# Optimization experiments

Measured on AMD Instinct MI355X. Metric: run time of the kernel, lower is better.

## Reference

```python
import jax, jax.numpy as jnp
import numpy as np

B, S, D, H, Dh, F = 1, 2048, 2048, 24, 128, 8192  # batch, seq, dim, heads, dim_head, ff hidden
SCALE = Dh ** -0.5


def _layernorm(x, g, b, eps=1e-5):
    mu = jnp.mean(x, axis=-1, keepdims=True)
    var = jnp.var(x, axis=-1, keepdims=True)
    return (x - mu) * jax.lax.rsqrt(var + eps) * g + b


def _rmsnorm(x, g, eps=1e-5):
    ms = jnp.mean(jnp.square(x), axis=-1, keepdims=True)
    return x * jax.lax.rsqrt(ms + eps) * g


def setup_inputs() -> dict:
    key = jax.random.key(0)
    ks = jax.random.split(key, 8)
    w = lambda k, sh: (jax.random.normal(k, sh, jnp.float32) * (1.0 / np.sqrt(sh[0]))).astype(jnp.float32)
    return {
        "x": jax.random.normal(ks[0], (B, S, D), jnp.float32),
        "ln_g": jnp.ones((D,), jnp.float32),
        "ln_b": jnp.zeros((D,), jnp.float32),
        "attn_g": jnp.ones((D,), jnp.float32),  # RingAttention prenorm (RMSNorm) gamma
        "Wq": w(ks[1], (D, H * Dh)),
        "Wk": w(ks[2], (D, H * Dh)),
        "Wv": w(ks[3], (D, H * Dh)),
        "Wo": w(ks[4], (H * Dh, D)),
        "W1": w(ks[5], (D, F)),
        "b1": jnp.zeros((F,), jnp.float32),
        "W2": w(ks[6], (F, D)),
        "b2": jnp.zeros((D,), jnp.float32),
    }


def reference(x, ln_g, ln_b, attn_g, Wq, Wk, Wv, Wo, W1, b1, W2, b2):
    # outer block LayerNorm
    x = _layernorm(x, ln_g, ln_b)

    # --- causal multi-head attention (math-equivalent to ring attention) ---
    h = _rmsnorm(x, attn_g)  # attention's internal prenorm
    q = (h @ Wq).reshape(B, S, H, Dh)
    k = (h @ Wk).reshape(B, S, H, Dh)
    v = (h @ Wv).reshape(B, S, H, Dh)
    scores = jnp.einsum("bqhd,bkhd->bhqk", q, k) * SCALE  # [B,H,S,S]
    causal = jnp.tril(jnp.ones((S, S), bool))
    scores = jnp.where(causal, scores, jnp.finfo(scores.dtype).min)
    attn = jax.nn.softmax(scores, axis=-1)
    o = jnp.einsum("bhqk,bkhd->bqhd", attn, v).reshape(B, S, H * Dh)
    x = o @ Wo + x  # residual

    # --- feedforward + residual ---
    x = jax.nn.gelu(x @ W1 + b1) @ W2 + b2 + x
    return x
```

## Files before the change

kernel.cpp:

```cpp
#include <hip/hip_runtime.h>
#include <hip/hip_bf16.h>

#define Sq 2048
#define Dm 2048
#define HDim 3072
#define QKVDim 9216
#define NH 24
#define DH 128
#define FF 8192
#define ATT_SCALE 0.08838834764831845f

using bf16 = __hip_bfloat16;
typedef __attribute__((ext_vector_type(8))) short bf16x8;
typedef __attribute__((ext_vector_type(4))) float f32x4;
typedef unsigned int u32;
typedef unsigned long long u64;
typedef __attribute__((ext_vector_type(4))) u32 u32x4;

__device__ __forceinline__ void gload_lds16(const void* g, void* l) {
    __builtin_amdgcn_global_load_lds(
        (const __attribute__((address_space(1))) void*)g,
        (__attribute__((address_space(3))) void*)l, 16, 0, 0);
}

__global__ __launch_bounds__(256) void ln_rms_kernel(
    const float* __restrict__ x, const float* __restrict__ g, const float* __restrict__ b,
    const float* __restrict__ ag, float* __restrict__ xnf, bf16* __restrict__ h)
{
    __shared__ float redA[4], redB[4], redC[4];
    int row = blockIdx.x;
    int t = threadIdx.x;
    int lane = t & 63, wid = t >> 6;
    const float* xr = x + (size_t)row * Dm;

    float v[8];
    float sum = 0.f, ssq = 0.f;
#pragma unroll
    for (int i = 0; i < 8; i++) {
        float f = xr[t + 256 * i];
        v[i] = f; sum += f; ssq += f * f;
    }
#pragma unroll
    for (int off = 32; off > 0; off >>= 1) {
        sum += __shfl_down(sum, off);
        ssq += __shfl_down(ssq, off);
    }
    if (lane == 0) { redA[wid] = sum; redB[wid] = ssq; }
    __syncthreads();
    sum = redA[0] + redA[1] + redA[2] + redA[3];
    ssq = redB[0] + redB[1] + redB[2] + redB[3];
    float mu = sum * (1.f / Dm);
    float var = ssq * (1.f / Dm) - mu * mu;
    float rstd = rsqrtf(var + 1e-5f);

    float xn[8];
    float s2 = 0.f;
#pragma unroll
    for (int i = 0; i < 8; i++) {
        int col = t + 256 * i;
        float xv = (v[i] - mu) * rstd * g[col] + b[col];
        xn[i] = xv;
        xnf[(size_t)row * Dm + col] = xv;
        s2 += xv * xv;
    }
#pragma unroll
    for (int off = 32; off > 0; off >>= 1) s2 += __shfl_down(s2, off);
    if (lane == 0) redC[wid] = s2;
    __syncthreads();
    s2 = redC[0] + redC[1] + redC[2] + redC[3];
    float rms = rsqrtf(s2 * (1.f / Dm) + 1e-5f);
#pragma unroll
    for (int i = 0; i < 8; i++) {
        int col = t + 256 * i;
        h[(size_t)row * Dm + col] = __float2bfloat16(xn[i] * rms * ag[col]);
    }
}

__global__ __launch_bounds__(256) void transpose_cvt_kernel(
    const float* __restrict__ W, bf16* __restrict__ Wt, int K, int N)
{
    __shared__ float tile[32][36];
    int n0 = blockIdx.x * 32, k0 = blockIdx.y * 32;
    int t = threadIdx.x;
    int r = t >> 3, c4 = (t & 7) * 4;
    f32x4 v = *reinterpret_cast<const f32x4*>(W + (size_t)(k0 + r) * N + n0 + c4);
    *reinterpret_cast<f32x4*>(&tile[r][c4]) = v;
    __syncthreads();
    int nr = t >> 3, kc = (t & 7) * 4;
    bf16 o4[4];
    o4[0] = __float2bfloat16(tile[kc + 0][nr]);
    o4[1] = __float2bfloat16(tile[kc + 1][nr]);
    o4[2] = __float2bfloat16(tile[kc + 2][nr]);
    o4[3] = __float2bfloat16(tile[kc + 3][nr]);
    *reinterpret_cast<u64*>(Wt + (size_t)(n0 + nr) * K + k0 + kc) = *reinterpret_cast<const u64*>(o4);
}

__global__ __launch_bounds__(256) void transpose_cvt3_kernel(
    const float* __restrict__ Wa, const float* __restrict__ Wb, const float* __restrict__ Wc,
    bf16* __restrict__ Wt, int K, int N)
{
    __shared__ float tile[32][36];
    const float* W = blockIdx.z == 0 ? Wa : (blockIdx.z == 1 ? Wb : Wc);
    bf16* dst = Wt + (size_t)blockIdx.z * N * K;
    int n0 = blockIdx.x * 32, k0 = blockIdx.y * 32;
    int t = threadIdx.x;
    int r = t >> 3, c4 = (t & 7) * 4;
    f32x4 v = *reinterpret_cast<const f32x4*>(W + (size_t)(k0 + r) * N + n0 + c4);
    *reinterpret_cast<f32x4*>(&tile[r][c4]) = v;
    __syncthreads();
    int nr = t >> 3, kc = (t & 7) * 4;
    bf16 o4[4];
    o4[0] = __float2bfloat16(tile[kc + 0][nr]);
    o4[1] = __float2bfloat16(tile[kc + 1][nr]);
    o4[2] = __float2bfloat16(tile[kc + 2][nr]);
    o4[3] = __float2bfloat16(tile[kc + 3][nr]);
    *reinterpret_cast<u64*>(dst + (size_t)(n0 + nr) * K + k0 + kc) = *reinterpret_cast<const u64*>(o4);
}

__global__ __launch_bounds__(256) void cvt_prefill_kernel(
    const float* __restrict__ xnf, const float* __restrict__ bias,
    bf16* __restrict__ hb, float* __restrict__ o, int N)
{
    int i = (blockIdx.x * 256 + threadIdx.x) * 8;
    int col = i % N;
    f32x4 a = *reinterpret_cast<const f32x4*>(xnf + i);
    f32x4 b = *reinterpret_cast<const f32x4*>(xnf + i + 4);
    bf16 r[8];
#pragma unroll
    for (int j = 0; j < 4; j++) { r[j] = __float2bfloat16(a[j]); r[4 + j] = __float2bfloat16(b[j]); }
    *reinterpret_cast<u32x4*>(hb + i) = *reinterpret_cast<const u32x4*>(r);
    f32x4 b0 = *reinterpret_cast<const f32x4*>(bias + col);
    f32x4 b1v = *reinterpret_cast<const f32x4*>(bias + col + 4);
    f32x4 o0 = {a[0] + b0[0], a[1] + b0[1], a[2] + b0[2], a[3] + b0[3]};
    f32x4 o1 = {b[0] + b1v[0], b[1] + b1v[1], b[2] + b1v[2], b[3] + b1v[3]};
    *reinterpret_cast<f32x4*>(o + i) = o0;
    *reinterpret_cast<f32x4*>(o + i + 4) = o1;
}

template <int EPI>
__global__ __launch_bounds__(256, 4) void gemm_kernel(
    const bf16* __restrict__ A, const bf16* __restrict__ Bt,
    int M, int N, int K, int Ksplit,
    bf16* Cb, float* Cf, const float* __restrict__ bias)
{
    __shared__ __align__(16) bf16 As[128 * 64];
    __shared__ __align__(16) bf16 Bs[128 * 64];
    int m0 = blockIdx.y * 128, n0 = blockIdx.x * 128;
    int kbeg = blockIdx.z * Ksplit, kend = kbeg + Ksplit;
    int tid = threadIdx.x;
    int lane = tid & 63, w = tid >> 6;
    int wr = w >> 1, wc = w & 1;
    int l15 = lane & 15, lhi = lane >> 4;

    int srow = lane >> 3;
    int scol = ((lane & 7) ^ (lane >> 3)) * 8;

    const f32x4 zero4 = {0.f, 0.f, 0.f, 0.f};
    f32x4 acc[4][4];
#pragma unroll
    for (int m = 0; m < 4; m++)
#pragma unroll
        for (int n = 0; n < 4; n++) acc[m][n] = zero4;

    for (int k0 = kbeg; k0 < kend; k0 += 64) {
        __syncthreads();
#pragma unroll
        for (int c = 0; c < 4; c++) {
            int row = w * 32 + c * 8 + srow;
            gload_lds16(A + (size_t)(m0 + row) * K + k0 + scol,
                        (char*)As + w * 4096 + c * 1024);
            gload_lds16(Bt + (size_t)(n0 + row) * K + k0 + scol,
                        (char*)Bs + w * 4096 + c * 1024);
        }
        __syncthreads();
#pragma unroll
        for (int ks = 0; ks < 2; ks++) {
            bf16x8 af[4], bfr[4];
#pragma unroll
            for (int m = 0; m < 4; m++) {
                int r = wr * 64 + m * 16 + l15;
                af[m] = *reinterpret_cast<const bf16x8*>(
                    &As[r * 64 + (((ks << 2) + lhi) ^ (r & 7)) * 8]);
            }
#pragma unroll
            for (int n = 0; n < 4; n++) {
                int r = wc * 64 + n * 16 + l15;
                bfr[n] = *reinterpret_cast<const bf16x8*>(
                    &Bs[r * 64 + (((ks << 2) + lhi) ^ (r & 7)) * 8]);
            }
#pragma unroll
            for (int m = 0; m < 4; m++)
#pragma unroll
                for (int n = 0; n < 4; n++)
                    acc[m][n] = __builtin_amdgcn_mfma_f32_16x16x32_bf16(af[m], bfr[n], acc[m][n], 0, 0, 0);
        }
    }

#pragma unroll
    for (int m = 0; m < 4; m++) {
        int row = m0 + wr * 64 + m * 16 + lhi * 4;
#pragma unroll
        for (int n = 0; n < 4; n++) {
            int col = n0 + wc * 64 + n * 16 + l15;
#pragma unroll
            for (int j = 0; j < 4; j++) {
                float vv = acc[m][n][j];
                size_t idx = (size_t)(row + j) * N + col;
                if (EPI == 0) {
                    Cb[idx] = __float2bfloat16(vv);
                } else if (EPI == 2) {
                    float o = vv + bias[col];
                    float u = 1.5957691216057308f * (o + 0.044715f * o * o * o);
                    Cb[idx] = __float2bfloat16(o / (1.0f + __expf(-u)));
                } else {
                    atomicAdd(&Cf[idx], vv);
                }
            }
        }
    }
}

__global__ __launch_bounds__(256) void attn_kernel(
    const bf16* __restrict__ qkv, bf16* __restrict__ o)
{
    __shared__ __align__(16) bf16 KsF[2][64 * 128];
    __shared__ __align__(16) bf16 VtF[2][128 * 72];
    __shared__ __align__(16) bf16 Pl[4][16][72];
    int rank = blockIdx.x;
    int qb = (Sq / 128 - 1) - rank / NH;
    int head = rank % NH;
    const bf16* q = qkv + head * DH;
    const bf16* k = qkv + HDim + head * DH;
    const bf16* v = qkv + 2 * HDim + head * DH;
    int tid = threadIdx.x, lane = tid & 63, w = tid >> 6;
    int l15 = lane & 15, lhi = lane >> 4;

    bf16x8 aq[2][4];
#pragma unroll
    for (int s = 0; s < 2; s++) {
        const bf16* qbase = q + (size_t)(qb * 128 + s * 64 + w * 16 + l15) * QKVDim;
#pragma unroll
        for (int kk = 0; kk < 4; kk++)
            aq[s][kk] = *reinterpret_cast<const bf16x8*>(qbase + kk * 32 + lhi * 8);
    }

    int krow_st = w * 16;
    int vkv = lhi * 2 + (w & 1) + (w >> 1) * 8;
    int vd0 = l15 * 8;
    int vxr = l15 & 7;

    const f32x4 zero4 = {0.f, 0.f, 0.f, 0.f};
    f32x4 acc_o[2][8];
    float mrow[2][4], lrow[2][4];
#pragma unroll
    for (int s = 0; s < 2; s++) {
#pragma unroll
        for (int db = 0; db < 8; db++) acc_o[s][db] = zero4;
#pragma unroll
        for (int r = 0; r < 4; r++) { mrow[s][r] = -1e30f; lrow[s][r] = 0.f; }
    }

    int nt = 2 * qb + 2;

    {
#pragma unroll
        for (int c = 0; c < 4; c++) {
            int row = krow_st + c * 4 + lhi;
            int cb = l15 ^ (row & 7);
            gload_lds16(k + (size_t)row * QKVDim + cb * 8,
                        (char*)&KsF[0][0] + w * 4096 + c * 1024);
        }
#pragma unroll
        for (int i = 0; i < 4; i++) {
            int kv = vkv + i * 16;
            bf16x8 vv = *reinterpret_cast<const bf16x8*>(v + (size_t)kv * QKVDim + vd0);
            int vb = kv >> 3, kr = kv & 7;
#pragma unroll
            for (int j = 0; j < 8; j++)
                VtF[0][(vd0 + j) * 72 + ((vb ^ vxr) << 3) + kr] = ((const bf16*)&vv)[j];
        }
        asm volatile("s_waitcnt vmcnt(0)" ::: "memory");
        __syncthreads();
    }

    for (int kb = 0; kb < nt; kb++) {
        int kv0 = kb * 64;
        int p = kb & 1;
        bf16x8 vreg[4];
        bool pref = (kb + 1 < nt);
        if (pref) {
            int nv0 = kv0 + 64;
#pragma unroll
            for (int c = 0; c < 4; c++) {
                int row = krow_st + c * 4 + lhi;
                int cb = l15 ^ (row & 7);
                gload_lds16(k + (size_t)(nv0 + row) * QKVDim + cb * 8,
                            (char*)&KsF[p ^ 1][0] + w * 4096 + c * 1024);
            }
#pragma unroll
            for (int i = 0; i < 4; i++) {
                int kv = vkv + i * 16;
                vreg[i] = *reinterpret_cast<const bf16x8*>(v + (size_t)(nv0 + kv) * QKVDim + vd0);
            }
        }

#pragma unroll
        for (int s = 0; s < 2; s++) {
            int qr0s = qb * 128 + s * 64 + w * 16;
            if (kv0 > qr0s + 15) continue;

            f32x4 sacc[4];
#pragma unroll
            for (int nb = 0; nb < 4; nb++) {
                sacc[nb] = zero4;
                int krow = nb * 16 + l15;
#pragma unroll
                for (int kk = 0; kk < 4; kk++) {
                    const char* kp = (const char*)&KsF[p][0] + krow * 256 +
                                     ((kk * 64 + lhi * 16) ^ ((krow & 7) << 4));
                    bf16x8 bk = *reinterpret_cast<const bf16x8*>(kp);
                    sacc[nb] = __builtin_amdgcn_mfma_f32_16x16x32_bf16(aq[s][kk], bk, sacc[nb], 0, 0, 0);
                }
            }

            bool msk = (kv0 + 63 > qr0s);
            float sv[4][4];
            float pm[4];
#pragma unroll
            for (int r = 0; r < 4; r++) pm[r] = -1e30f;
#pragma unroll
            for (int nb = 0; nb < 4; nb++) {
                int kvc = kv0 + nb * 16 + l15;
#pragma unroll
                for (int r = 0; r < 4; r++) {
                    int qr = qr0s + lhi * 4 + r;
                    float ss = sacc[nb][r] * ATT_SCALE;
                    if (msk && kvc > qr) ss = -1e30f;
                    sv[nb][r] = ss;
                    pm[r] = fmaxf(pm[r], ss);
                }
            }
#pragma unroll
            for (int off = 1; off < 16; off <<= 1)
#pragma unroll
                for (int r = 0; r < 4; r++)
                    pm[r] = fmaxf(pm[r], __shfl_xor(pm[r], off));

            float ls[4];
#pragma unroll
            for (int r = 0; r < 4; r++) {
                float mnew = fmaxf(mrow[s][r], pm[r]);
                float sc = __expf(mrow[s][r] - mnew);
                mrow[s][r] = mnew;
                lrow[s][r] *= sc;
#pragma unroll
                for (int db = 0; db < 8; db++) acc_o[s][db][r] *= sc;
                float lsr = 0.f;
#pragma unroll
                for (int nb = 0; nb < 4; nb++) {
                    float pp = __expf(sv[nb][r] - mnew);
                    sv[nb][r] = pp;
                    lsr += pp;
                }
                ls[r] = lsr;
            }
#pragma unroll
            for (int off = 1; off < 16; off <<= 1)
#pragma unroll
                for (int r = 0; r < 4; r++)
                    ls[r] += __shfl_xor(ls[r], off);
#pragma unroll
            for (int r = 0; r < 4; r++) lrow[s][r] += ls[r];

#pragma unroll
            for (int nb = 0; nb < 4; nb++)
#pragma unroll
                for (int r = 0; r < 4; r++)
                    Pl[w][lhi * 4 + r][nb * 16 + l15] = __float2bfloat16(sv[nb][r]);

#pragma unroll
            for (int ks = 0; ks < 2; ks++) {
                bf16x8 ap = *reinterpret_cast<const bf16x8*>(&Pl[w][l15][ks * 32 + lhi * 8]);
#pragma unroll
                for (int db = 0; db < 8; db++) {
                    int dv = db * 16 + l15;
                    int blk = (ks * 4 + lhi) ^ ((dv >> 3) & 7);
                    bf16x8 bv = *reinterpret_cast<const bf16x8*>(&VtF[p][dv * 72 + blk * 8]);
                    acc_o[s][db] = __builtin_amdgcn_mfma_f32_16x16x32_bf16(ap, bv, acc_o[s][db], 0, 0, 0);
                }
            }
        }

        __syncthreads();
        if (pref) {
            int nv0 = kv0 + 64;
            (void)nv0;
#pragma unroll
            for (int i = 0; i < 4; i++) {
                int kv = vkv + i * 16;
                int vb = kv >> 3, kr = kv & 7;
#pragma unroll
                for (int j = 0; j < 8; j++)
                    VtF[p ^ 1][(vd0 + j) * 72 + ((vb ^ vxr) << 3) + kr] = ((const bf16*)&vreg[i])[j];
            }
            asm volatile("s_waitcnt vmcnt(0)" ::: "memory");
            __syncthreads();
        }
    }

#pragma unroll
    for (int s = 0; s < 2; s++)
#pragma unroll
        for (int db = 0; db < 8; db++)
#pragma unroll
            for (int r = 0; r < 4; r++) {
                int qr = qb * 128 + s * 64 + w * 16 + lhi * 4 + r;
                float val = acc_o[s][db][r] / lrow[s][r];
                o[(size_t)qr * HDim + head * DH + db * 16 + l15] = __float2bfloat16(val);
            }
}

extern "C" void kernel_launch(void* const* d_in, const int* in_sizes, int n_in,
                              void* d_out, int out_size, void* d_ws, size_t ws_size,
                              hipStream_t stream)
{
    const float* x     = (const float*)d_in[0];
    const float* ln_g  = (const float*)d_in[1];
    const float* ln_b  = (const float*)d_in[2];
    const float* attng = (const float*)d_in[3];
    const float* Wq    = (const float*)d_in[4];
    const float* Wk    = (const float*)d_in[5];
    const float* Wv    = (const float*)d_in[6];
    const float* Wo    = (const float*)d_in[7];
    const float* W1    = (const float*)d_in[8];
    const float* b1    = (const float*)d_in[9];
    const float* W2    = (const float*)d_in[10];
    const float* b2    = (const float*)d_in[11];
    float* out = (float*)d_out;
    char* ws = (char*)d_ws;

    bf16*  wbuf = (bf16*)(ws + 0);
    float* xnf  = (float*)(ws + 39845888);
    bf16*  hbuf = (bf16*)(ws + 56623104);
    bf16*  qkv  = (bf16*)(ws + 65011712);
    bf16*  ob_  = (bf16*)(ws + 102760448);
    bf16*  gb_  = qkv;

    ln_rms_kernel<<<Sq, 256, 0, stream>>>(x, ln_g, ln_b, attng, xnf, hbuf);

    transpose_cvt3_kernel<<<dim3(HDim / 32, Dm / 32, 3), 256, 0, stream>>>(
        Wq, Wk, Wv, wbuf, Dm, HDim);
    gemm_kernel<0><<<dim3(QKVDim / 128, Sq / 128, 1), 256, 0, stream>>>(
        hbuf, wbuf, Sq, QKVDim, Dm, Dm, qkv, nullptr, nullptr);

    attn_kernel<<<dim3(NH * Sq / 128), 256, 0, stream>>>(qkv, ob_);

    transpose_cvt_kernel<<<dim3(Dm / 32, HDim / 32), 256, 0, stream>>>(Wo, wbuf, HDim, Dm);
    gemm_kernel<4><<<dim3(Dm / 128, Sq / 128, 2), 256, 0, stream>>>(
        ob_, wbuf, Sq, Dm, HDim, HDim / 2, nullptr, xnf, nullptr);
    cvt_prefill_kernel<<<(Sq * Dm) / (256 * 8), 256, 0, stream>>>(xnf, b2, hbuf, out, Dm);

    transpose_cvt_kernel<<<dim3(FF / 32, Dm / 32), 256, 0, stream>>>(W1, wbuf, Dm, FF);
    gemm_kernel<2><<<dim3(FF / 128, Sq / 128, 1), 256, 0, stream>>>(
        hbuf, wbuf, Sq, FF, Dm, Dm, gb_, nullptr, b1);

    transpose_cvt_kernel<<<dim3(Dm / 32, FF / 32), 256, 0, stream>>>(W2, wbuf, FF, Dm);
    gemm_kernel<4><<<dim3(Dm / 128, Sq / 128, 2), 256, 0, stream>>>(
        gb_, wbuf, Sq, Dm, FF, FF / 2, nullptr, out, nullptr);
}
```

Measured before the change: 502.6 us.

## Shrink attention query tile to 64 and load K fragments directly to registers

The attention kernel now processes 64 query rows per block instead of 128, doubling the grid. K tiles are no longer staged through LDS; each wave loads its MFMA B-fragments straight from global memory into registers, prefetching the next tile after the QK MFMAs. This removes the K LDS buffer and its waits and improves occupancy and load balance. The cost is that every wave reads the full K tile from global/L2, so K traffic rises, and each KV tile is reused by half as many queries.

```diff
diff --git a/kernel.cpp b/kernel.cpp
--- a/kernel.cpp
+++ b/kernel.cpp
@@ -223,201 +223,177 @@
 __global__ __launch_bounds__(256) void attn_kernel(
     const bf16* __restrict__ qkv, bf16* __restrict__ o)
 {
-    __shared__ __align__(16) bf16 KsF[2][64 * 128];
     __shared__ __align__(16) bf16 VtF[2][128 * 72];
     __shared__ __align__(16) bf16 Pl[4][16][72];
     int rank = blockIdx.x;
-    int qb = (Sq / 128 - 1) - rank / NH;
+    int qb = (Sq / 64 - 1) - rank / NH;
     int head = rank % NH;
     const bf16* q = qkv + head * DH;
     const bf16* k = qkv + HDim + head * DH;
     const bf16* v = qkv + 2 * HDim + head * DH;
     int tid = threadIdx.x, lane = tid & 63, w = tid >> 6;
     int l15 = lane & 15, lhi = lane >> 4;
-
-    bf16x8 aq[2][4];
-#pragma unroll
-    for (int s = 0; s < 2; s++) {
-        const bf16* qbase = q + (size_t)(qb * 128 + s * 64 + w * 16 + l15) * QKVDim;
-#pragma unroll
-        for (int kk = 0; kk < 4; kk++)
-            aq[s][kk] = *reinterpret_cast<const bf16x8*>(qbase + kk * 32 + lhi * 8);
-    }
-
-    int krow_st = w * 16;
+    int qrow0 = qb * 64 + w * 16;
+
+    bf16x8 aq[4];
+    const bf16* qbase = q + (size_t)(qrow0 + l15) * QKVDim;
+#pragma unroll
+    for (int kk = 0; kk < 4; kk++)
+        aq[kk] = *reinterpret_cast<const bf16x8*>(qbase + kk * 32 + lhi * 8);
+
+    const bf16* kbase = k + (size_t)l15 * QKVDim + lhi * 8;
+
     int vkv = lhi * 2 + (w & 1) + (w >> 1) * 8;
     int vd0 = l15 * 8;
     int vxr = l15 & 7;
+    const bf16* vbase = v + (size_t)vkv * QKVDim + vd0;
 
     const f32x4 zero4 = {0.f, 0.f, 0.f, 0.f};
-    f32x4 acc_o[2][8];
-    float mrow[2][4], lrow[2][4];
-#pragma unroll
-    for (int s = 0; s < 2; s++) {
-#pragma unroll
-        for (int db = 0; db < 8; db++) acc_o[s][db] = zero4;
-#pragma unroll
-        for (int r = 0; r < 4; r++) { mrow[s][r] = -1e30f; lrow[s][r] = 0.f; }
-    }
-
-    int nt = 2 * qb + 2;
-
-    {
-#pragma unroll
-        for (int c = 0; c < 4; c++) {
-            int row = krow_st + c * 4 + lhi;
-            int cb = l15 ^ (row & 7);
-            gload_lds16(k + (size_t)row * QKVDim + cb * 8,
-                        (char*)&KsF[0][0] + w * 4096 + c * 1024);
-        }
-#pragma unroll
-        for (int i = 0; i < 4; i++) {
-            int kv = vkv + i * 16;
-            bf16x8 vv = *reinterpret_cast<const bf16x8*>(v + (size_t)kv * QKVDim + vd0);
-            int vb = kv >> 3, kr = kv & 7;
-#pragma unroll
-            for (int j = 0; j < 8; j++)
-                VtF[0][(vd0 + j) * 72 + ((vb ^ vxr) << 3) + kr] = ((const bf16*)&vv)[j];
-        }
-        asm volatile("s_waitcnt vmcnt(0)" ::: "memory");
-        __syncthreads();
-    }
+    f32x4 acc_o[8];
+#pragma unroll
+    for (int db = 0; db < 8; db++) acc_o[db] = zero4;
+    float mrow[4], lrow[4];
+#pragma unroll
+    for (int r = 0; r < 4; r++) { mrow[r] = -1e30f; lrow[r] = 0.f; }
+
+    int nt = qb + 1;
+    bf16x8 bk[4][4], vreg[4];
+
+#pragma unroll
+    for (int nb = 0; nb < 4; nb++)
+#pragma unroll
+        for (int kk = 0; kk < 4; kk++)
+            bk[nb][kk] = *reinterpret_cast<const bf16x8*>(
+                kbase + (size_t)(nb * 16) * QKVDim + kk * 32);
+#pragma unroll
+    for (int i = 0; i < 4; i++)
+        vreg[i] = *reinterpret_cast<const bf16x8*>(vbase + (size_t)(i * 16) * QKVDim);
+#pragma unroll
+    for (int i = 0; i < 4; i++) {
+        int kv = vkv + i * 16, vb = kv >> 3, kr = kv & 7;
+#pragma unroll
+        for (int j = 0; j < 8; j++)
+            VtF[0][(vd0 + j) * 72 + ((vb ^ vxr) << 3) + kr] = ((const bf16*)&vreg[i])[j];
+    }
+    __syncthreads();
 
     for (int kb = 0; kb < nt; kb++) {
-        int kv0 = kb * 64;
-        int p = kb & 1;
-        bf16x8 vreg[4];
+        int kv0 = kb * 64, p = kb & 1;
         bool pref = (kb + 1 < nt);
+        size_t nref = (size_t)(kv0 + 64) * QKVDim;
         if (pref) {
-            int nv0 = kv0 + 64;
-#pragma unroll
-            for (int c = 0; c < 4; c++) {
-                int row = krow_st + c * 4 + lhi;
-                int cb = l15 ^ (row & 7);
-                gload_lds16(k + (size_t)(nv0 + row) * QKVDim + cb * 8,
-                            (char*)&KsF[p ^ 1][0] + w * 4096 + c * 1024);
-            }
-#pragma unroll
-            for (int i = 0; i < 4; i++) {
-                int kv = vkv + i * 16;
-                vreg[i] = *reinterpret_cast<const bf16x8*>(v + (size_t)(nv0 + kv) * QKVDim + vd0);
-            }
-        }
-
-#pragma unroll
-        for (int s = 0; s < 2; s++) {
-            int qr0s = qb * 128 + s * 64 + w * 16;
-            if (kv0 > qr0s + 15) continue;
-
-            f32x4 sacc[4];
+#pragma unroll
+            for (int i = 0; i < 4; i++)
+                vreg[i] = *reinterpret_cast<const bf16x8*>(
+                    vbase + nref + (size_t)(i * 16) * QKVDim);
+        }
+
+        f32x4 sacc[4];
+#pragma unroll
+        for (int nb = 0; nb < 4; nb++) {
+            sacc[nb] = zero4;
+#pragma unroll
+            for (int kk = 0; kk < 4; kk++)
+                sacc[nb] = __builtin_amdgcn_mfma_f32_16x16x32_bf16(aq[kk], bk[nb][kk], sacc[nb], 0, 0, 0);
+        }
+
+        if (pref) {
+#pragma unroll
+            for (int nb = 0; nb < 4; nb++)
+#pragma unroll
+                for (int kk = 0; kk < 4; kk++)
+                    bk[nb][kk] = *reinterpret_cast<const bf16x8*>(
+                        kbase + nref + (size_t)(nb * 16) * QKVDim + kk * 32);
+        }
+
+        bool diag = (kb == qb);
+        float sv[4][4];
+        float pm[4];
+#pragma unroll
+        for (int r = 0; r < 4; r++) pm[r] = -1e30f;
+#pragma unroll
+        for (int nb = 0; nb < 4; nb++) {
+            int kvc = kv0 + nb * 16 + l15;
+#pragma unroll
+            for (int r = 0; r < 4; r++) {
+                int qr = qrow0 + lhi * 4 + r;
+                float s = sacc[nb][r] * ATT_SCALE;
+                if (diag && kvc > qr) s = -1e30f;
+                sv[nb][r] = s;
+                pm[r] = fmaxf(pm[r], s);
+            }
+        }
+#pragma unroll
+        for (int off = 1; off < 16; off <<= 1)
+#pragma unroll
+            for (int r = 0; r < 4; r++)
+                pm[r] = fmaxf(pm[r], __shfl_xor(pm[r], off));
+
+        float ls[4];
+#pragma unroll
+        for (int r = 0; r < 4; r++) {
+            float mnew = fmaxf(mrow[r], pm[r]);
+            float sc = __expf(mrow[r] - mnew);
+            mrow[r] = mnew;
+            lrow[r] *= sc;
+#pragma unroll
+            for (int db = 0; db < 8; db++) acc_o[db][r] *= sc;
+            float lsr = 0.f;
 #pragma unroll
             for (int nb = 0; nb < 4; nb++) {
-                sacc[nb] = zero4;
-                int krow = nb * 16 + l15;
-#pragma unroll
-                for (int kk = 0; kk < 4; kk++) {
-                    const char* kp = (const char*)&KsF[p][0] + krow * 256 +
-                                     ((kk * 64 + lhi * 16) ^ ((krow & 7) << 4));
-                    bf16x8 bk = *reinterpret_cast<const bf16x8*>(kp);
-                    sacc[nb] = __builtin_amdgcn_mfma_f32_16x16x32_bf16(aq[s][kk], bk, sacc[nb], 0, 0, 0);
-                }
-            }
-
-            bool msk = (kv0 + 63 > qr0s);
-            float sv[4][4];
-            float pm[4];
-#pragma unroll
-            for (int r = 0; r < 4; r++) pm[r] = -1e30f;
-#pragma unroll
-            for (int nb = 0; nb < 4; nb++) {
-                int kvc = kv0 + nb * 16 + l15;
-#pragma unroll
-                for (int r = 0; r < 4; r++) {
-                    int qr = qr0s + lhi * 4 + r;
-                    float ss = sacc[nb][r] * ATT_SCALE;
-                    if (msk && kvc > qr) ss = -1e30f;
-                    sv[nb][r] = ss;
-                    pm[r] = fmaxf(pm[r], ss);
-                }
-            }
-#pragma unroll
-            for (int off = 1; off < 16; off <<= 1)
-#pragma unroll
-                for (int r = 0; r < 4; r++)
-                    pm[r] = fmaxf(pm[r], __shfl_xor(pm[r], off));
-
-            float ls[4];
-#pragma unroll
-            for (int r = 0; r < 4; r++) {
-                float mnew = fmaxf(mrow[s][r], pm[r]);
-                float sc = __expf(mrow[s][r] - mnew);
-                mrow[s][r] = mnew;
-                lrow[s][r] *= sc;
-#pragma unroll
-                for (int db = 0; db < 8; db++) acc_o[s][db][r] *= sc;
-                float lsr = 0.f;
-#pragma unroll
-                for (int nb = 0; nb < 4; nb++) {
-                    float pp = __expf(sv[nb][r] - mnew);
-                    sv[nb][r] = pp;
-                    lsr += pp;
-                }
-                ls[r] = lsr;
-            }
-#pragma unroll
-            for (int off = 1; off < 16; off <<= 1)
-#pragma unroll
-                for (int r = 0; r < 4; r++)
-                    ls[r] += __shfl_xor(ls[r], off);
-#pragma unroll
-            for (int r = 0; r < 4; r++) lrow[s][r] += ls[r];
-
-#pragma unroll
-            for (int nb = 0; nb < 4; nb++)
-#pragma unroll
-                for (int r = 0; r < 4; r++)
-                    Pl[w][lhi * 4 + r][nb * 16 + l15] = __float2bfloat16(sv[nb][r]);
-
-#pragma unroll
-            for (int ks = 0; ks < 2; ks++) {
-                bf16x8 ap = *reinterpret_cast<const bf16x8*>(&Pl[w][l15][ks * 32 + lhi * 8]);
-#pragma unroll
-                for (int db = 0; db < 8; db++) {
-                    int dv = db * 16 + l15;
-                    int blk = (ks * 4 + lhi) ^ ((dv >> 3) & 7);
-                    bf16x8 bv = *reinterpret_cast<const bf16x8*>(&VtF[p][dv * 72 + blk * 8]);
-                    acc_o[s][db] = __builtin_amdgcn_mfma_f32_16x16x32_bf16(ap, bv, acc_o[s][db], 0, 0, 0);
-                }
+                float pp = __expf(sv[nb][r] - mnew);
+                sv[nb][r] = pp;
+                lsr += pp;
+            }
+            ls[r] = lsr;
+        }
+#pragma unroll
+        for (int off = 1; off < 16; off <<= 1)
+#pragma unroll
+            for (int r = 0; r < 4; r++)
+                ls[r] += __shfl_xor(ls[r], off);
+#pragma unroll
+        for (int r = 0; r < 4; r++) lrow[r] += ls[r];
+
+#pragma unroll
+        for (int nb = 0; nb < 4; nb++)
+#pragma unroll
+            for (int r = 0; r < 4; r++)
+                Pl[w][lhi * 4 + r][nb * 16 + l15] = __float2bfloat16(sv[nb][r]);
+
+#pragma unroll
+        for (int ks = 0; ks < 2; ks++) {
+            bf16x8 ap = *reinterpret_cast<const bf16x8*>(&Pl[w][l15][ks * 32 + lhi * 8]);
+#pragma unroll
+            for (int db = 0; db < 8; db++) {
+                int dv = db * 16 + l15;
+                int blk = (ks * 4 + lhi) ^ ((dv >> 3) & 7);
+                bf16x8 bv = *reinterpret_cast<const bf16x8*>(&VtF[p][dv * 72 + blk * 8]);
+                acc_o[db] = __builtin_amdgcn_mfma_f32_16x16x32_bf16(ap, bv, acc_o[db], 0, 0, 0);
             }
         }
 
         __syncthreads();
         if (pref) {
-            int nv0 = kv0 + 64;
-            (void)nv0;
 #pragma unroll
             for (int i = 0; i < 4; i++) {
-                int kv = vkv + i * 16;
-                int vb = kv >> 3, kr = kv & 7;
+                int kv = vkv + i * 16, vb = kv >> 3, kr = kv & 7;
 #pragma unroll
                 for (int j = 0; j < 8; j++)
                     VtF[p ^ 1][(vd0 + j) * 72 + ((vb ^ vxr) << 3) + kr] = ((const bf16*)&vreg[i])[j];
             }
-            asm volatile("s_waitcnt vmcnt(0)" ::: "memory");
             __syncthreads();
         }
     }
 
 #pragma unroll
-    for (int s = 0; s < 2; s++)
-#pragma unroll
-        for (int db = 0; db < 8; db++)
-#pragma unroll
-            for (int r = 0; r < 4; r++) {
-                int qr = qb * 128 + s * 64 + w * 16 + lhi * 4 + r;
-                float val = acc_o[s][db][r] / lrow[s][r];
-                o[(size_t)qr * HDim + head * DH + db * 16 + l15] = __float2bfloat16(val);
-            }
+    for (int db = 0; db < 8; db++)
+#pragma unroll
+        for (int r = 0; r < 4; r++) {
+            int qr = qrow0 + lhi * 4 + r;
+            float val = acc_o[db][r] / lrow[r];
+            o[(size_t)qr * HDim + head * DH + db * 16 + l15] = __float2bfloat16(val);
+        }
 }
 
 extern "C" void kernel_launch(void* const* d_in, const int* in_sizes, int n_in,
@@ -453,7 +429,7 @@
     gemm_kernel<0><<<dim3(QKVDim / 128, Sq / 128, 1), 256, 0, stream>>>(
         hbuf, wbuf, Sq, QKVDim, Dm, Dm, qkv, nullptr, nullptr);
 
-    attn_kernel<<<dim3(NH * Sq / 128), 256, 0, stream>>>(qkv, ob_);
+    attn_kernel<<<dim3(NH * Sq / 64), 256, 0, stream>>>(qkv, ob_);
 
     transpose_cvt_kernel<<<dim3(Dm / 32, HDim / 32), 256, 0, stream>>>(Wo, wbuf, HDim, Dm);
     gemm_kernel<4><<<dim3(Dm / 128, Sq / 128, 2), 256, 0, stream>>>(
```

Result: no change. 493.3 us (-1.9%).
